# Optimization experiments

Measured on AMD Instinct MI355X. Metric: run time of the kernel, lower is better.

Reference implementation:

```python
import jax, jax.numpy as jnp
import numpy as np

FORGET_BIAS = 1.0  # tf.nn.rnn_cell.LSTMCell default


def _lstm_scan(x_btE, W, b, hidden):
    """x: (B,T,E). W: (E+H, 4H), gate order i, j, f, o (TF LSTMCell)."""
    B = x_btE.shape[0]
    h0 = jnp.zeros((B, hidden), x_btE.dtype)
    c0 = jnp.zeros((B, hidden), x_btE.dtype)

    def step(carry, x_t):
        h, c = carry
        z = jnp.concatenate([x_t, h], axis=-1) @ W + b  # (B, 4H)
        i, j, f, o = jnp.split(z, 4, axis=-1)
        c_new = jax.nn.sigmoid(f + FORGET_BIAS) * c + jax.nn.sigmoid(i) * jnp.tanh(j)
        h_new = jax.nn.sigmoid(o) * jnp.tanh(c_new)
        return (h_new, c_new), h_new

    (_, _), hs = jax.lax.scan(step, (h0, c0), jnp.swapaxes(x_btE, 0, 1))
    return jnp.swapaxes(hs, 0, 1)  # (B, T, H)


def setup_inputs() -> dict:
    key = jax.random.key(0)
    ks = jax.random.split(key, 5)
    B, T, V, E, H, C = 256, 120, 50000, 256, 1024, 5
    tokens = jax.random.randint(ks[0], (B, T, 1), 0, V, dtype=jnp.int32)
    embeddings = jax.random.normal(ks[1], (V, E), jnp.float32) * 0.1
    W_lstm = jax.random.normal(ks[2], (E + H, 4 * H), jnp.float32) * (1.0 / np.sqrt(E + H))
    b_lstm = jnp.zeros((4 * H,), jnp.float32)
    U = jax.random.normal(ks[3], (H, C), jnp.float32) * (1.0 / np.sqrt(H))
    b2 = jnp.zeros((C,), jnp.float32)
    return {"tokens": tokens, "embeddings": embeddings, "W_lstm": W_lstm,
            "b_lstm": b_lstm, "U": U, "b2": b2}


def reference(tokens, embeddings, W_lstm, b_lstm, U, b2):
    B, T, F = tokens.shape  # F == n_features == 1
    E = embeddings.shape[1]
    H = U.shape[0]
    # embedding lookup + reshape to (B, T, F*E)
    x = embeddings[tokens].reshape(B, T, F * E)
    outputs = _lstm_scan(x, W_lstm, b_lstm, H)  # (B, T, H); dropout keep_prob=1 -> identity
    preds = outputs.reshape(-1, H) @ U + b2
    return preds.reshape(B, T, -1)  # (B, max_length, n_classes)
```

## Files before the change

### kernel.cpp

```cpp
#include <hip/hip_runtime.h>

typedef unsigned short u16;
typedef unsigned int u32;
typedef unsigned long long u64;
typedef int   v4i  __attribute__((ext_vector_type(4)));
typedef short v8s  __attribute__((ext_vector_type(8)));
typedef float v2f  __attribute__((ext_vector_type(2)));
typedef float v16f __attribute__((ext_vector_type(16)));

#define B_ 256
#define T_ 120
#define E_ 256
#define H_ 1024
#define K_ 1280
#define LDH 1032
#define LDX 264

#define WS_WF   0
#define WS_X    10485760
#define WS_HS   26214400
#define WS_BAR  89128960

__device__ __forceinline__ u16 f2bf(float f) {
    union { float f; u32 u; } v; v.f = f;
    u32 r = v.u + 0x7fffu + ((v.u >> 16) & 1u);
    return (u16)(r >> 16);
}
__device__ __forceinline__ float bf2f(u16 u) {
    union { u32 u; float f; } v; v.u = ((u32)u) << 16; return v.f;
}
__device__ __forceinline__ float fsig(float x) {
    float t = __builtin_amdgcn_exp2f(-1.44269504f * x);
    return __builtin_amdgcn_rcpf(1.0f + t);
}
__device__ __forceinline__ float ftanh_(float x) {
    float xc = fminf(8.0f, fmaxf(-8.0f, x));
    float t = __builtin_amdgcn_exp2f(2.88539008f * xc);
    return (t - 1.0f) * __builtin_amdgcn_rcpf(t + 1.0f);
}
__device__ __forceinline__ void gl_lds16(const void* g, void* l) {
    __builtin_amdgcn_global_load_lds(
        (const __attribute__((address_space(1))) void*)g,
        (__attribute__((address_space(3))) void*)l, 16, 0, 0);
}

__global__ void prep_w(const float* __restrict__ W, u16* __restrict__ Wf) {
    __shared__ u16 tile[32 * 136];
    int bid = blockIdx.x;
    int cid = bid / 5, fo = bid % 5;
    int kh  = cid & 1, g = (cid >> 1) & 3, nc = cid >> 3;
    int colbase = g * 1024 + nc * 32;
    int tid = threadIdx.x;
    int c = tid & 31, r = tid >> 5;

#pragma unroll
    for (int fl = 0; fl < 8; ++fl) {
        int k0 = (2 * (fo * 8 + fl) + kh) * 16;
#pragma unroll
        for (int rr = 0; rr < 2; ++rr) {
            int row = r + rr * 8;
            float v = W[(size_t)(k0 + row) * 4096 + colbase + c];
            tile[c * 136 + fl * 16 + row] = f2bf(v);
        }
    }
    __syncthreads();

    int lane = tid & 63;
#pragma unroll
    for (int pass = 0; pass < 2; ++pass) {
        int fl = (tid >> 6) + pass * 4;
        v4i o = *(const v4i*)&tile[(lane & 31) * 136 + fl * 16 + ((lane >> 5) << 3)];
        *(v4i*)(Wf + (((size_t)(cid * 40 + fo * 8 + fl)) << 9) + lane * 8) = o;
    }
}

__global__ void prep_x(const int* __restrict__ tokens, const float* __restrict__ emb,
                       u16* __restrict__ X) {
    int v   = blockIdx.x * 256 + threadIdx.x;
    int e8  = v & 31;
    int row = v >> 5;
    int t = row >> 8, b = row & 255;
    int tok = tokens[b * T_ + t];
    const float* src = emb + (size_t)tok * E_ + e8 * 8;
    u16 o[8];
#pragma unroll
    for (int j = 0; j < 8; ++j) o[j] = f2bf(src[j]);
    *(v4i*)(X + (size_t)row * E_ + e8 * 8) = *(v4i*)o;
}

__global__ __launch_bounds__(512, 2) void lstm_main(
    const u16* __restrict__ Wf, const u16* __restrict__ X,
    const float* __restrict__ b_lstm, u16* __restrict__ hs,
    u32* __restrict__ bar) {

    __shared__ u16  hbuf[32 * LDH];
    __shared__ u16  xbuf[32 * LDX];
    __shared__ float gates[2 * 4 * 32 * 34];
    __shared__ float bias[128];

    const int tid   = threadIdx.x;
    const int lane  = tid & 63;
    const int wv    = tid >> 6;
    const int g     = wv >> 1;
    const int khalf = wv & 1;
    const int bid   = blockIdx.x;
    const int mchunk = bid & 7;
    const int nc    = bid >> 3;
    const int m0    = mchunk << 5;

    if (tid < 128) bias[tid] = b_lstm[(tid >> 5) * H_ + (nc << 5) + (tid & 31)];

    v8s Wr[40];
    {
        const int cid = nc * 8 + g * 2 + khalf;
        const v4i* wsrc = (const v4i*)(Wf + (size_t)cid * 40 * 512);
#pragma unroll
        for (int f = 0; f < 40; ++f)
            Wr[f] = __builtin_bit_cast(v8s, wsrc[f * 64 + lane]);
    }
#pragma unroll
    for (int f = 0; f < 40; ++f) asm volatile("" : "+v"(Wr[f]));

    {
        const v4i* xs = (const v4i*)(X + (size_t)m0 * E_);
#pragma unroll
        for (int i = 0; i < 2; ++i) {
            int idx = tid + i * 512;
            int r = idx >> 5, c8 = idx & 31;
            *(v4i*)&xbuf[r * LDX + c8 * 8] = xs[r * 32 + c8];
        }
    }
    __syncthreads();

    const u16* Ax = &xbuf[(lane & 31) * LDX + ((lane >> 5) << 3)];
    const u16* Ah = &hbuf[(lane & 31) * LDH + ((lane >> 5) << 3)];

    v16f acc = {0,0,0,0,0,0,0,0,0,0,0,0,0,0,0,0};
#pragma unroll
    for (int f = 0; f < 8; ++f) {
        v8s a = *(const v8s*)(Ax + (2 * f + khalf) * 16);
        acc = __builtin_amdgcn_mfma_f32_32x32x16_bf16(a, Wr[f], acc, 0, 0, 0);
    }

    float cst[2] = {0.f, 0.f};
    const int cm  = tid >> 4;
    const int cn2 = (tid & 15) << 1;
    u32* hs32 = (u32*)hs;

    for (int t = 0; t < T_; ++t) {
        if (t > 0) {
            if (tid == 0) {
                u32* p = &bar[mchunk * T_ + (t - 1)];
                while (__hip_atomic_load(p, __ATOMIC_RELAXED, __HIP_MEMORY_SCOPE_AGENT) < 32u)
                    __builtin_amdgcn_s_sleep(1);
            }
            __syncthreads();
            {
                const u16* srcb = hs + ((size_t)(t - 1) * B_ + m0) * H_;
                int r0 = wv << 2;
#pragma unroll
                for (int half = 0; half < 2; ++half)
#pragma unroll
                    for (int i = 0; i < 4; ++i) {
                        int r = r0 + i;
                        gl_lds16(srcb + (size_t)r * H_ + half * 512 + lane * 8,
                                 &hbuf[r * LDH + half * 512]);
                    }
            }
            asm volatile("s_waitcnt vmcnt(4)\n\ts_barrier" ::: "memory");
#pragma unroll
            for (int f = 8; f < 24; ++f) {
                v8s a = *(const v8s*)(Ah + ((2 * f + khalf) * 16 - 256));
                acc = __builtin_amdgcn_mfma_f32_32x32x16_bf16(a, Wr[f], acc, 0, 0, 0);
            }
            asm volatile("s_waitcnt vmcnt(0)\n\ts_barrier" ::: "memory");
#pragma unroll
            for (int f = 24; f < 40; ++f) {
                v8s a = *(const v8s*)(Ah + ((2 * f + khalf) * 16 - 256));
                acc = __builtin_amdgcn_mfma_f32_32x32x16_bf16(a, Wr[f], acc, 0, 0, 0);
            }
        }

        {
            float* gb = &gates[((khalf << 2) + g) * 1088];
            int col = lane & 31, rq = (lane >> 5) << 2;
#pragma unroll
            for (int reg = 0; reg < 16; ++reg) {
                int row = (reg & 3) + ((reg >> 2) << 3) + rq;
                gb[row * 34 + col] = acc[reg];
            }
        }
        __syncthreads();

        if (t + 1 < T_) {
            const v4i* xs = (const v4i*)(X + ((size_t)(t + 1) * B_ + m0) * E_);
#pragma unroll
            for (int i = 0; i < 2; ++i) {
                int idx = tid + i * 512;
                int r = idx >> 5, c8 = idx & 31;
                *(v4i*)&xbuf[r * LDX + c8 * 8] = xs[r * 32 + c8];
            }
        }

        u32 hpack = 0;
        {
            v2f zz[4];
#pragma unroll
            for (int gg = 0; gg < 4; ++gg) {
                v2f a = *(const v2f*)&gates[gg * 1088 + cm * 34 + cn2];
                v2f b = *(const v2f*)&gates[(4 + gg) * 1088 + cm * 34 + cn2];
                zz[gg].x = a.x + b.x; zz[gg].y = a.y + b.y;
            }
#pragma unroll
            for (int q = 0; q < 2; ++q) {
                int n = cn2 + q;
                float ip = zz[0][q] + bias[n];
                float jp = zz[1][q] + bias[32 + n];
                float fp = zz[2][q] + bias[64 + n] + 1.0f;
                float op = zz[3][q] + bias[96 + n];
                float cc = fsig(fp) * cst[q] + fsig(ip) * ftanh_(jp);
                cst[q] = cc;
                hpack |= ((u32)f2bf(fsig(op) * ftanh_(cc))) << (16 * q);
            }
        }
        __hip_atomic_store(&hs32[((size_t)t * B_ + m0 + cm) * 512 + (nc << 4) + (tid & 15)],
                           hpack, __ATOMIC_RELAXED, __HIP_MEMORY_SCOPE_AGENT);

        if (t + 1 < T_) {
            asm volatile("s_waitcnt vmcnt(0)" ::: "memory");
            __syncthreads();
            if (tid == 0)
                __hip_atomic_fetch_add(&bar[mchunk * T_ + t], 1u,
                                       __ATOMIC_RELAXED, __HIP_MEMORY_SCOPE_AGENT);
#pragma unroll
            for (int reg = 0; reg < 16; ++reg) acc[reg] = 0.f;
#pragma unroll
            for (int f = 0; f < 8; ++f) {
                v8s a = *(const v8s*)(Ax + (2 * f + khalf) * 16);
                acc = __builtin_amdgcn_mfma_f32_32x32x16_bf16(a, Wr[f], acc, 0, 0, 0);
            }
        }
    }
}

__global__ void proj_kernel(const u16* __restrict__ hs, const float* __restrict__ U,
                            const float* __restrict__ b2, float* __restrict__ out) {
    __shared__ float Ul[H_ * 5];
    int tid = threadIdx.x;
    for (int i = tid; i < H_ * 5; i += 256) Ul[i] = U[i];
    __syncthreads();
    int wv = tid >> 6, lane = tid & 63;
#pragma unroll 1
    for (int i = 0; i < 16; ++i) {
        int row = blockIdx.x * 64 + wv * 16 + i;
        int t = row >> 8, b = row & 255;
        const v4i* hp = (const v4i*)(hs + (size_t)row * H_);
        float p[5] = {0.f, 0.f, 0.f, 0.f, 0.f};
#pragma unroll
        for (int half = 0; half < 2; ++half) {
            v4i hv = hp[lane * 2 + half];
            u16 us[8];
            *(v4i*)us = hv;
#pragma unroll
            for (int j = 0; j < 8; ++j) {
                float hf = bf2f(us[j]);
                int k = lane * 16 + half * 8 + j;
#pragma unroll
                for (int c = 0; c < 5; ++c) p[c] += hf * Ul[k * 5 + c];
            }
        }
#pragma unroll
        for (int c = 0; c < 5; ++c)
            for (int off = 32; off > 0; off >>= 1)
                p[c] += __shfl_down(p[c], off, 64);
        if (lane == 0) {
#pragma unroll
            for (int c = 0; c < 5; ++c)
                out[((size_t)b * T_ + t) * 5 + c] = p[c] + b2[c];
        }
    }
}

extern "C" void kernel_launch(void* const* d_in, const int* in_sizes, int n_in,
                              void* d_out, int out_size, void* d_ws, size_t ws_size,
                              hipStream_t stream) {
    const int*   tokens = (const int*)d_in[0];
    const float* emb    = (const float*)d_in[1];
    const float* W      = (const float*)d_in[2];
    const float* b_l    = (const float*)d_in[3];
    const float* U      = (const float*)d_in[4];
    const float* b2     = (const float*)d_in[5];
    float* out = (float*)d_out;

    char* ws = (char*)d_ws;
    u16* Wf  = (u16*)(ws + WS_WF);
    u16* X   = (u16*)(ws + WS_X);
    u16* hs  = (u16*)(ws + WS_HS);
    u32* bar = (u32*)(ws + WS_BAR);

    hipMemsetAsync(bar, 0, 8 * T_ * sizeof(u32), stream);
    prep_w<<<1280, 256, 0, stream>>>(W, Wf);
    prep_x<<<3840, 256, 0, stream>>>(tokens, emb, X);
    lstm_main<<<256, 512, 0, stream>>>(Wf, X, b_l, hs, bar);
    proj_kernel<<<480, 256, 0, stream>>>(hs, U, b2, out);
}
```

Measured before the change: 607.9 us.

## Split LSTM step barrier into per-half flags and restructure wave K/N split

Each wave now owns two gate column tiles and a quarter of K instead of one gate and half of K, so the prepacked weight layout and the gate reduction change to four partial sums. The per-timestep barrier counter is split into two flags, one per half of the hidden dimension, so each block can start loading the first half of h while the second half is still being produced. The input-projection MFMAs are moved to after the wait, overlapping with the asynchronous h loads. This aims to shorten the serial critical path per step, at the cost of more LDS for gate partials and every thread spin-polling the flags instead of a single thread.

```diff
diff --git a/kernel.cpp b/kernel.cpp
--- a/kernel.cpp
+++ b/kernel.cpp
@@ -45,32 +45,33 @@
 }
 
 __global__ void prep_w(const float* __restrict__ W, u16* __restrict__ Wf) {
-    __shared__ u16 tile[32 * 136];
+    __shared__ u16 tile[64 * 72];
     int bid = blockIdx.x;
     int cid = bid / 5, fo = bid % 5;
-    int kh  = cid & 1, g = (cid >> 1) & 3, nc = cid >> 3;
-    int colbase = g * 1024 + nc * 32;
+    int kq  = cid & 3, np = (cid >> 2) & 1, nc = cid >> 3;
     int tid = threadIdx.x;
-    int c = tid & 31, r = tid >> 5;
-
-#pragma unroll
-    for (int fl = 0; fl < 8; ++fl) {
-        int k0 = (2 * (fo * 8 + fl) + kh) * 16;
-#pragma unroll
-        for (int rr = 0; rr < 2; ++rr) {
-            int row = r + rr * 8;
-            float v = W[(size_t)(k0 + row) * 4096 + colbase + c];
-            tile[c * 136 + fl * 16 + row] = f2bf(v);
+    int cc = tid & 31, n = (tid >> 5) & 1, r = tid >> 6;
+
+    int col = (np * 2 + n) * 1024 + nc * 32 + cc;
+#pragma unroll
+    for (int fl = 0; fl < 4; ++fl) {
+        int k0 = (4 * (fo * 4 + fl) + kq) * 16;
+#pragma unroll
+        for (int rr = 0; rr < 4; ++rr) {
+            int krow = rr * 4 + r;
+            float v = W[(size_t)(k0 + krow) * 4096 + col];
+            tile[(n * 32 + cc) * 72 + fl * 16 + krow] = f2bf(v);
         }
     }
     __syncthreads();
 
-    int lane = tid & 63;
+    int lane = tid & 63, wvv = tid >> 6;
 #pragma unroll
     for (int pass = 0; pass < 2; ++pass) {
-        int fl = (tid >> 6) + pass * 4;
-        v4i o = *(const v4i*)&tile[(lane & 31) * 136 + fl * 16 + ((lane >> 5) << 3)];
-        *(v4i*)(Wf + (((size_t)(cid * 40 + fo * 8 + fl)) << 9) + lane * 8) = o;
+        int slot = wvv + pass * 4;
+        int fl = slot >> 1, nn = slot & 1;
+        v4i o = *(const v4i*)&tile[(nn * 32 + (lane & 31)) * 72 + fl * 16 + ((lane >> 5) << 3)];
+        *(v4i*)(Wf + (size_t)cid * 20480 + (((fo * 4 + fl) * 2 + nn) << 9) + lane * 8) = o;
     }
 }
 
@@ -95,31 +96,36 @@
 
     __shared__ u16  hbuf[32 * LDH];
     __shared__ u16  xbuf[32 * LDX];
-    __shared__ float gates[2 * 4 * 32 * 34];
+    __shared__ float gates[4 * 4 * 32 * 34];
     __shared__ float bias[128];
 
     const int tid   = threadIdx.x;
     const int lane  = tid & 63;
     const int wv    = tid >> 6;
-    const int g     = wv >> 1;
-    const int khalf = wv & 1;
+    const int np    = wv >> 2;
+    const int kq    = wv & 3;
     const int bid   = blockIdx.x;
     const int mchunk = bid & 7;
     const int nc    = bid >> 3;
     const int m0    = mchunk << 5;
+    const int hl    = nc >> 4;
 
     if (tid < 128) bias[tid] = b_lstm[(tid >> 5) * H_ + (nc << 5) + (tid & 31)];
 
-    v8s Wr[40];
+    v8s Wr[20][2];
     {
-        const int cid = nc * 8 + g * 2 + khalf;
-        const v4i* wsrc = (const v4i*)(Wf + (size_t)cid * 40 * 512);
-#pragma unroll
-        for (int f = 0; f < 40; ++f)
-            Wr[f] = __builtin_bit_cast(v8s, wsrc[f * 64 + lane]);
-    }
-#pragma unroll
-    for (int f = 0; f < 40; ++f) asm volatile("" : "+v"(Wr[f]));
+        const v4i* wsrc = (const v4i*)(Wf + (size_t)(nc * 8 + np * 4 + kq) * 20480);
+#pragma unroll
+        for (int f = 0; f < 20; ++f)
+#pragma unroll
+            for (int n = 0; n < 2; ++n)
+                Wr[f][n] = __builtin_bit_cast(v8s, wsrc[(f * 2 + n) * 64 + lane]);
+    }
+#pragma unroll
+    for (int f = 0; f < 20; ++f) {
+        asm volatile("" : "+v"(Wr[f][0]));
+        asm volatile("" : "+v"(Wr[f][1]));
+    }
 
     {
         const v4i* xs = (const v4i*)(X + (size_t)m0 * E_);
@@ -135,59 +141,69 @@
     const u16* Ax = &xbuf[(lane & 31) * LDX + ((lane >> 5) << 3)];
     const u16* Ah = &hbuf[(lane & 31) * LDH + ((lane >> 5) << 3)];
 
-    v16f acc = {0,0,0,0,0,0,0,0,0,0,0,0,0,0,0,0};
-#pragma unroll
-    for (int f = 0; f < 8; ++f) {
-        v8s a = *(const v8s*)(Ax + (2 * f + khalf) * 16);
-        acc = __builtin_amdgcn_mfma_f32_32x32x16_bf16(a, Wr[f], acc, 0, 0, 0);
-    }
-
     float cst[2] = {0.f, 0.f};
     const int cm  = tid >> 4;
     const int cn2 = (tid & 15) << 1;
     u32* hs32 = (u32*)hs;
 
     for (int t = 0; t < T_; ++t) {
+        v16f acc0 = {0,0,0,0,0,0,0,0,0,0,0,0,0,0,0,0};
+        v16f acc1 = {0,0,0,0,0,0,0,0,0,0,0,0,0,0,0,0};
+
         if (t > 0) {
-            if (tid == 0) {
-                u32* p = &bar[mchunk * T_ + (t - 1)];
-                while (__hip_atomic_load(p, __ATOMIC_RELAXED, __HIP_MEMORY_SCOPE_AGENT) < 32u)
-                    __builtin_amdgcn_s_sleep(1);
-            }
-            __syncthreads();
-            {
-                const u16* srcb = hs + ((size_t)(t - 1) * B_ + m0) * H_;
-                int r0 = wv << 2;
-#pragma unroll
-                for (int half = 0; half < 2; ++half)
-#pragma unroll
-                    for (int i = 0; i < 4; ++i) {
-                        int r = r0 + i;
-                        gl_lds16(srcb + (size_t)r * H_ + half * 512 + lane * 8,
-                                 &hbuf[r * LDH + half * 512]);
-                    }
+            const u32* flg = &bar[((size_t)mchunk * T_ + (t - 1)) * 2];
+            const u16* srcb = hs + ((size_t)(t - 1) * B_ + m0) * H_;
+            const int r0 = wv << 2;
+            while (__hip_atomic_load(&flg[0], __ATOMIC_RELAXED, __HIP_MEMORY_SCOPE_AGENT) < 16u)
+                __builtin_amdgcn_s_sleep(1);
+#pragma unroll
+            for (int i = 0; i < 4; ++i)
+                gl_lds16(srcb + (size_t)(r0 + i) * H_ + lane * 8,
+                         &hbuf[(r0 + i) * LDH]);
+            while (__hip_atomic_load(&flg[1], __ATOMIC_RELAXED, __HIP_MEMORY_SCOPE_AGENT) < 16u)
+                __builtin_amdgcn_s_sleep(1);
+#pragma unroll
+            for (int i = 0; i < 4; ++i)
+                gl_lds16(srcb + (size_t)(r0 + i) * H_ + 512 + lane * 8,
+                         &hbuf[(r0 + i) * LDH + 512]);
+#pragma unroll
+            for (int f = 0; f < 4; ++f) {
+                v8s a = *(const v8s*)(Ax + (4 * f + kq) * 16);
+                acc0 = __builtin_amdgcn_mfma_f32_32x32x16_bf16(a, Wr[f][0], acc0, 0, 0, 0);
+                acc1 = __builtin_amdgcn_mfma_f32_32x32x16_bf16(a, Wr[f][1], acc1, 0, 0, 0);
             }
             asm volatile("s_waitcnt vmcnt(4)\n\ts_barrier" ::: "memory");
 #pragma unroll
-            for (int f = 8; f < 24; ++f) {
-                v8s a = *(const v8s*)(Ah + ((2 * f + khalf) * 16 - 256));
-                acc = __builtin_amdgcn_mfma_f32_32x32x16_bf16(a, Wr[f], acc, 0, 0, 0);
+            for (int f = 4; f < 12; ++f) {
+                v8s a = *(const v8s*)(Ah + (4 * f + kq) * 16 - 256);
+                acc0 = __builtin_amdgcn_mfma_f32_32x32x16_bf16(a, Wr[f][0], acc0, 0, 0, 0);
+                acc1 = __builtin_amdgcn_mfma_f32_32x32x16_bf16(a, Wr[f][1], acc1, 0, 0, 0);
             }
             asm volatile("s_waitcnt vmcnt(0)\n\ts_barrier" ::: "memory");
 #pragma unroll
-            for (int f = 24; f < 40; ++f) {
-                v8s a = *(const v8s*)(Ah + ((2 * f + khalf) * 16 - 256));
-                acc = __builtin_amdgcn_mfma_f32_32x32x16_bf16(a, Wr[f], acc, 0, 0, 0);
+            for (int f = 12; f < 20; ++f) {
+                v8s a = *(const v8s*)(Ah + (4 * f + kq) * 16 - 256);
+                acc0 = __builtin_amdgcn_mfma_f32_32x32x16_bf16(a, Wr[f][0], acc0, 0, 0, 0);
+                acc1 = __builtin_amdgcn_mfma_f32_32x32x16_bf16(a, Wr[f][1], acc1, 0, 0, 0);
+            }
+        } else {
+#pragma unroll
+            for (int f = 0; f < 4; ++f) {
+                v8s a = *(const v8s*)(Ax + (4 * f + kq) * 16);
+                acc0 = __builtin_amdgcn_mfma_f32_32x32x16_bf16(a, Wr[f][0], acc0, 0, 0, 0);
+                acc1 = __builtin_amdgcn_mfma_f32_32x32x16_bf16(a, Wr[f][1], acc1, 0, 0, 0);
             }
         }
 
         {
-            float* gb = &gates[((khalf << 2) + g) * 1088];
             int col = lane & 31, rq = (lane >> 5) << 2;
+            float* g0 = &gates[(kq * 4 + np * 2 + 0) * 1088];
+            float* g1 = &gates[(kq * 4 + np * 2 + 1) * 1088];
 #pragma unroll
             for (int reg = 0; reg < 16; ++reg) {
                 int row = (reg & 3) + ((reg >> 2) << 3) + rq;
-                gb[row * 34 + col] = acc[reg];
+                g0[row * 34 + col] = acc0[reg];
+                g1[row * 34 + col] = acc1[reg];
             }
         }
         __syncthreads();
@@ -207,9 +223,12 @@
             v2f zz[4];
 #pragma unroll
             for (int gg = 0; gg < 4; ++gg) {
-                v2f a = *(const v2f*)&gates[gg * 1088 + cm * 34 + cn2];
-                v2f b = *(const v2f*)&gates[(4 + gg) * 1088 + cm * 34 + cn2];
-                zz[gg].x = a.x + b.x; zz[gg].y = a.y + b.y;
+                v2f s0 = *(const v2f*)&gates[(0 * 4 + gg) * 1088 + cm * 34 + cn2];
+                v2f s1 = *(const v2f*)&gates[(1 * 4 + gg) * 1088 + cm * 34 + cn2];
+                v2f s2 = *(const v2f*)&gates[(2 * 4 + gg) * 1088 + cm * 34 + cn2];
+                v2f s3 = *(const v2f*)&gates[(3 * 4 + gg) * 1088 + cm * 34 + cn2];
+                zz[gg].x = (s0.x + s1.x) + (s2.x + s3.x);
+                zz[gg].y = (s0.y + s1.y) + (s2.y + s3.y);
             }
 #pragma unroll
             for (int q = 0; q < 2; ++q) {
@@ -230,15 +249,8 @@
             asm volatile("s_waitcnt vmcnt(0)" ::: "memory");
             __syncthreads();
             if (tid == 0)
-                __hip_atomic_fetch_add(&bar[mchunk * T_ + t], 1u,
+                __hip_atomic_fetch_add(&bar[((size_t)mchunk * T_ + t) * 2 + hl], 1u,
                                        __ATOMIC_RELAXED, __HIP_MEMORY_SCOPE_AGENT);
-#pragma unroll
-            for (int reg = 0; reg < 16; ++reg) acc[reg] = 0.f;
-#pragma unroll
-            for (int f = 0; f < 8; ++f) {
-                v8s a = *(const v8s*)(Ax + (2 * f + khalf) * 16);
-                acc = __builtin_amdgcn_mfma_f32_32x32x16_bf16(a, Wr[f], acc, 0, 0, 0);
-            }
         }
     }
 }
@@ -298,7 +310,7 @@
     u16* hs  = (u16*)(ws + WS_HS);
     u32* bar = (u32*)(ws + WS_BAR);
 
-    hipMemsetAsync(bar, 0, 8 * T_ * sizeof(u32), stream);
+    hipMemsetAsync(bar, 0, 8 * T_ * 2 * sizeof(u32), stream);
     prep_w<<<1280, 256, 0, stream>>>(W, Wf);
     prep_x<<<3840, 256, 0, stream>>>(tokens, emb, X);
     lstm_main<<<256, 512, 0, stream>>>(Wf, X, b_l, hs, bar);
```

New measurement: 1.201 ms. 97.6% more time.

## Fuse projection into LSTM kernel, merge prep kernels, use per-block barrier flags

Applied to the files above, without the earlier changes.

Merges the weight, embedding and output-bias prep into one launch, and removes the separate projection kernel. Each block now projects its h slice onto U in registers and accumulates into the output with atomicAdd, which avoids re-reading all hidden states. The inter-block barrier changes from one counter with atomic adds to 32 per-producer flags that 32 threads poll in parallel. This adds global atomics and an unconditional barrier plus vmcnt wait on every step, and the order of the float atomic sums is nondeterministic.

```diff
diff --git a/kernel.cpp b/kernel.cpp
--- a/kernel.cpp
+++ b/kernel.cpp
@@ -12,7 +12,6 @@
 #define T_ 120
 #define E_ 256
 #define H_ 1024
-#define K_ 1280
 #define LDH 1032
 #define LDX 264
 
@@ -26,9 +25,6 @@
     u32 r = v.u + 0x7fffu + ((v.u >> 16) & 1u);
     return (u16)(r >> 16);
 }
-__device__ __forceinline__ float bf2f(u16 u) {
-    union { u32 u; float f; } v; v.u = ((u32)u) << 16; return v.f;
-}
 __device__ __forceinline__ float fsig(float x) {
     float t = __builtin_amdgcn_exp2f(-1.44269504f * x);
     return __builtin_amdgcn_rcpf(1.0f + t);
@@ -44,54 +40,61 @@
         (__attribute__((address_space(3))) void*)l, 16, 0, 0);
 }
 
-__global__ void prep_w(const float* __restrict__ W, u16* __restrict__ Wf) {
+__global__ void prep_all(const float* __restrict__ W, u16* __restrict__ Wf,
+                         const int* __restrict__ tokens, const float* __restrict__ emb,
+                         u16* __restrict__ X, const float* __restrict__ b2,
+                         float* __restrict__ out) {
     __shared__ u16 tile[32 * 136];
     int bid = blockIdx.x;
-    int cid = bid / 5, fo = bid % 5;
-    int kh  = cid & 1, g = (cid >> 1) & 3, nc = cid >> 3;
-    int colbase = g * 1024 + nc * 32;
     int tid = threadIdx.x;
-    int c = tid & 31, r = tid >> 5;
-
-#pragma unroll
-    for (int fl = 0; fl < 8; ++fl) {
-        int k0 = (2 * (fo * 8 + fl) + kh) * 16;
-#pragma unroll
-        for (int rr = 0; rr < 2; ++rr) {
-            int row = r + rr * 8;
-            float v = W[(size_t)(k0 + row) * 4096 + colbase + c];
-            tile[c * 136 + fl * 16 + row] = f2bf(v);
-        }
-    }
-    __syncthreads();
-
-    int lane = tid & 63;
-#pragma unroll
-    for (int pass = 0; pass < 2; ++pass) {
-        int fl = (tid >> 6) + pass * 4;
-        v4i o = *(const v4i*)&tile[(lane & 31) * 136 + fl * 16 + ((lane >> 5) << 3)];
-        *(v4i*)(Wf + (((size_t)(cid * 40 + fo * 8 + fl)) << 9) + lane * 8) = o;
-    }
-}
-
-__global__ void prep_x(const int* __restrict__ tokens, const float* __restrict__ emb,
-                       u16* __restrict__ X) {
-    int v   = blockIdx.x * 256 + threadIdx.x;
-    int e8  = v & 31;
-    int row = v >> 5;
-    int t = row >> 8, b = row & 255;
-    int tok = tokens[b * T_ + t];
-    const float* src = emb + (size_t)tok * E_ + e8 * 8;
-    u16 o[8];
-#pragma unroll
-    for (int j = 0; j < 8; ++j) o[j] = f2bf(src[j]);
-    *(v4i*)(X + (size_t)row * E_ + e8 * 8) = *(v4i*)o;
+    if (bid < 1280) {
+        int cid = bid / 5, fo = bid % 5;
+        int kh  = cid & 1, g = (cid >> 1) & 3, nc = cid >> 3;
+        int colbase = g * 1024 + nc * 32;
+        int c = tid & 31, r = tid >> 5;
+#pragma unroll
+        for (int fl = 0; fl < 8; ++fl) {
+            int k0 = (2 * (fo * 8 + fl) + kh) * 16;
+#pragma unroll
+            for (int rr = 0; rr < 2; ++rr) {
+                int row = r + rr * 8;
+                float v = W[(size_t)(k0 + row) * 4096 + colbase + c];
+                tile[c * 136 + fl * 16 + row] = f2bf(v);
+            }
+        }
+        __syncthreads();
+        int lane = tid & 63;
+#pragma unroll
+        for (int pass = 0; pass < 2; ++pass) {
+            int fl = (tid >> 6) + pass * 4;
+            v4i o = *(const v4i*)&tile[(lane & 31) * 136 + fl * 16 + ((lane >> 5) << 3)];
+            *(v4i*)(Wf + (((size_t)(cid * 40 + fo * 8 + fl)) << 9) + lane * 8) = o;
+        }
+    } else if (bid < 5120) {
+        int v   = (bid - 1280) * 256 + tid;
+        int e8  = v & 31;
+        int row = v >> 5;
+        int t = row >> 8, b = row & 255;
+        int tok = tokens[b * T_ + t];
+        const float* src = emb + (size_t)tok * E_ + e8 * 8;
+        u16 o[8];
+#pragma unroll
+        for (int j = 0; j < 8; ++j) o[j] = f2bf(src[j]);
+        *(v4i*)(X + (size_t)row * E_ + e8 * 8) = *(v4i*)o;
+    } else {
+        int row = (bid - 5120) * 256 + tid;
+        if (row < B_ * T_) {
+#pragma unroll
+            for (int c = 0; c < 5; ++c) out[(size_t)row * 5 + c] = b2[c];
+        }
+    }
 }
 
 __global__ __launch_bounds__(512, 2) void lstm_main(
     const u16* __restrict__ Wf, const u16* __restrict__ X,
     const float* __restrict__ b_lstm, u16* __restrict__ hs,
-    u32* __restrict__ bar) {
+    u32* __restrict__ bar, const float* __restrict__ U,
+    float* __restrict__ out) {
 
     __shared__ u16  hbuf[32 * LDH];
     __shared__ u16  xbuf[32 * LDX];
@@ -112,14 +115,22 @@
 
     v8s Wr[40];
     {
-        const int cid = nc * 8 + g * 2 + khalf;
-        const v4i* wsrc = (const v4i*)(Wf + (size_t)cid * 40 * 512);
+        const v4i* wsrc = (const v4i*)(Wf + (size_t)(nc * 8 + g * 2 + khalf) * 20480);
 #pragma unroll
         for (int f = 0; f < 40; ++f)
             Wr[f] = __builtin_bit_cast(v8s, wsrc[f * 64 + lane]);
     }
 #pragma unroll
     for (int f = 0; f < 40; ++f) asm volatile("" : "+v"(Wr[f]));
+
+    const int cm  = tid >> 4;
+    const int cn2 = (tid & 15) << 1;
+    float Ur[2][5];
+#pragma unroll
+    for (int q = 0; q < 2; ++q)
+#pragma unroll
+        for (int c = 0; c < 5; ++c)
+            Ur[q][c] = U[(size_t)((nc << 5) + cn2 + q) * 5 + c];
 
     {
         const v4i* xs = (const v4i*)(X + (size_t)m0 * E_);
@@ -143,46 +154,44 @@
     }
 
     float cst[2] = {0.f, 0.f};
-    const int cm  = tid >> 4;
-    const int cn2 = (tid & 15) << 1;
     u32* hs32 = (u32*)hs;
 
     for (int t = 0; t < T_; ++t) {
         if (t > 0) {
-            if (tid == 0) {
-                u32* p = &bar[mchunk * T_ + (t - 1)];
-                while (__hip_atomic_load(p, __ATOMIC_RELAXED, __HIP_MEMORY_SCOPE_AGENT) < 32u)
+            if (tid < 32) {
+                u32* p = &bar[(size_t)((mchunk * T_ + (t - 1)) << 5) + tid];
+                while (!__hip_atomic_load(p, __ATOMIC_RELAXED, __HIP_MEMORY_SCOPE_AGENT))
                     __builtin_amdgcn_s_sleep(1);
             }
             __syncthreads();
             {
                 const u16* srcb = hs + ((size_t)(t - 1) * B_ + m0) * H_;
-                int r0 = wv << 2;
-#pragma unroll
-                for (int half = 0; half < 2; ++half)
-#pragma unroll
-                    for (int i = 0; i < 4; ++i) {
-                        int r = r0 + i;
-                        gl_lds16(srcb + (size_t)r * H_ + half * 512 + lane * 8,
-                                 &hbuf[r * LDH + half * 512]);
-                    }
+                const int r0 = wv << 2;
+#pragma unroll
+                for (int i = 0; i < 4; ++i)
+                    gl_lds16(srcb + (size_t)(r0 + i) * H_ + lane * 8,
+                             &hbuf[(r0 + i) * LDH]);
+#pragma unroll
+                for (int i = 0; i < 4; ++i)
+                    gl_lds16(srcb + (size_t)(r0 + i) * H_ + 512 + lane * 8,
+                             &hbuf[(r0 + i) * LDH + 512]);
             }
             asm volatile("s_waitcnt vmcnt(4)\n\ts_barrier" ::: "memory");
 #pragma unroll
             for (int f = 8; f < 24; ++f) {
-                v8s a = *(const v8s*)(Ah + ((2 * f + khalf) * 16 - 256));
+                v8s a = *(const v8s*)(Ah + (2 * f + khalf) * 16 - 256);
                 acc = __builtin_amdgcn_mfma_f32_32x32x16_bf16(a, Wr[f], acc, 0, 0, 0);
             }
             asm volatile("s_waitcnt vmcnt(0)\n\ts_barrier" ::: "memory");
 #pragma unroll
             for (int f = 24; f < 40; ++f) {
-                v8s a = *(const v8s*)(Ah + ((2 * f + khalf) * 16 - 256));
+                v8s a = *(const v8s*)(Ah + (2 * f + khalf) * 16 - 256);
                 acc = __builtin_amdgcn_mfma_f32_32x32x16_bf16(a, Wr[f], acc, 0, 0, 0);
             }
         }
 
         {
-            float* gb = &gates[((khalf << 2) + g) * 1088];
+            float* gb = &gates[(khalf * 4 + g) * 1088];
             int col = lane & 31, rq = (lane >> 5) << 2;
 #pragma unroll
             for (int reg = 0; reg < 16; ++reg) {
@@ -202,7 +211,7 @@
             }
         }
 
-        u32 hpack = 0;
+        float hh[2];
         {
             v2f zz[4];
 #pragma unroll
@@ -211,6 +220,7 @@
                 v2f b = *(const v2f*)&gates[(4 + gg) * 1088 + cm * 34 + cn2];
                 zz[gg].x = a.x + b.x; zz[gg].y = a.y + b.y;
             }
+            u32 hpack = 0;
 #pragma unroll
             for (int q = 0; q < 2; ++q) {
                 int n = cn2 + q;
@@ -220,18 +230,19 @@
                 float op = zz[3][q] + bias[96 + n];
                 float cc = fsig(fp) * cst[q] + fsig(ip) * ftanh_(jp);
                 cst[q] = cc;
-                hpack |= ((u32)f2bf(fsig(op) * ftanh_(cc))) << (16 * q);
-            }
-        }
-        __hip_atomic_store(&hs32[((size_t)t * B_ + m0 + cm) * 512 + (nc << 4) + (tid & 15)],
-                           hpack, __ATOMIC_RELAXED, __HIP_MEMORY_SCOPE_AGENT);
-
+                hh[q] = fsig(op) * ftanh_(cc);
+                hpack |= ((u32)f2bf(hh[q])) << (16 * q);
+            }
+            __hip_atomic_store(&hs32[((size_t)t * B_ + m0 + cm) * 512 + (nc << 4) + (tid & 15)],
+                               hpack, __ATOMIC_RELAXED, __HIP_MEMORY_SCOPE_AGENT);
+        }
+
+        asm volatile("s_waitcnt vmcnt(0)" ::: "memory");
+        __syncthreads();
         if (t + 1 < T_) {
-            asm volatile("s_waitcnt vmcnt(0)" ::: "memory");
-            __syncthreads();
             if (tid == 0)
-                __hip_atomic_fetch_add(&bar[mchunk * T_ + t], 1u,
-                                       __ATOMIC_RELAXED, __HIP_MEMORY_SCOPE_AGENT);
+                __hip_atomic_store(&bar[(size_t)((mchunk * T_ + t) << 5) + nc], 1u,
+                                   __ATOMIC_RELAXED, __HIP_MEMORY_SCOPE_AGENT);
 #pragma unroll
             for (int reg = 0; reg < 16; ++reg) acc[reg] = 0.f;
 #pragma unroll
@@ -240,43 +251,25 @@
                 acc = __builtin_amdgcn_mfma_f32_32x32x16_bf16(a, Wr[f], acc, 0, 0, 0);
             }
         }
-    }
-}
-
-__global__ void proj_kernel(const u16* __restrict__ hs, const float* __restrict__ U,
-                            const float* __restrict__ b2, float* __restrict__ out) {
-    __shared__ float Ul[H_ * 5];
-    int tid = threadIdx.x;
-    for (int i = tid; i < H_ * 5; i += 256) Ul[i] = U[i];
-    __syncthreads();
-    int wv = tid >> 6, lane = tid & 63;
-#pragma unroll 1
-    for (int i = 0; i < 16; ++i) {
-        int row = blockIdx.x * 64 + wv * 16 + i;
-        int t = row >> 8, b = row & 255;
-        const v4i* hp = (const v4i*)(hs + (size_t)row * H_);
-        float p[5] = {0.f, 0.f, 0.f, 0.f, 0.f};
-#pragma unroll
-        for (int half = 0; half < 2; ++half) {
-            v4i hv = hp[lane * 2 + half];
-            u16 us[8];
-            *(v4i*)us = hv;
-#pragma unroll
-            for (int j = 0; j < 8; ++j) {
-                float hf = bf2f(us[j]);
-                int k = lane * 16 + half * 8 + j;
-#pragma unroll
-                for (int c = 0; c < 5; ++c) p[c] += hf * Ul[k * 5 + c];
-            }
-        }
-#pragma unroll
-        for (int c = 0; c < 5; ++c)
-            for (int off = 32; off > 0; off >>= 1)
-                p[c] += __shfl_down(p[c], off, 64);
-        if (lane == 0) {
+
+        {
+            float p[5];
 #pragma unroll
             for (int c = 0; c < 5; ++c)
-                out[((size_t)b * T_ + t) * 5 + c] = p[c] + b2[c];
+                p[c] = hh[0] * Ur[0][c] + hh[1] * Ur[1][c];
+#pragma unroll
+            for (int c = 0; c < 5; ++c) {
+                p[c] += __shfl_xor(p[c], 1, 16);
+                p[c] += __shfl_xor(p[c], 2, 16);
+                p[c] += __shfl_xor(p[c], 4, 16);
+                p[c] += __shfl_xor(p[c], 8, 16);
+            }
+            if ((tid & 15) == 0) {
+                float* dst = &out[((size_t)(m0 + cm) * T_ + t) * 5];
+#pragma unroll
+                for (int c = 0; c < 5; ++c)
+                    atomicAdd(dst + c, p[c]);
+            }
         }
     }
 }
@@ -298,9 +291,7 @@
     u16* hs  = (u16*)(ws + WS_HS);
     u32* bar = (u32*)(ws + WS_BAR);
 
-    hipMemsetAsync(bar, 0, 8 * T_ * sizeof(u32), stream);
-    prep_w<<<1280, 256, 0, stream>>>(W, Wf);
-    prep_x<<<3840, 256, 0, stream>>>(tokens, emb, X);
-    lstm_main<<<256, 512, 0, stream>>>(Wf, X, b_l, hs, bar);
-    proj_kernel<<<480, 256, 0, stream>>>(hs, U, b2, out);
-}
+    hipMemsetAsync(bar, 0, 8 * T_ * 32 * sizeof(u32), stream);
+    prep_all<<<5240, 256, 0, stream>>>(W, Wf, tokens, emb, X, b2, out);
+    lstm_main<<<256, 512, 0, stream>>>(Wf, X, b_l, hs, bar, U, out);
+}
```

New measurement: 928.7 us. 52.8% more time.

## Replace atomic-counter barrier with per-block flags and merge prep kernels

Applied to the files above, without the earlier changes.

The per-step grid barrier now uses one flag slot per producer block, set with plain atomic stores, and 32 threads each poll one flag. This replaces a single counter hit by 32 atomic fetch-adds. The memset and the two prep kernels are folded into one prep_all launch that also zeroes the enlarged flag array, removing two launches. The cost is more flag memory and wider polling traffic in each step.

```diff
diff --git a/kernel.cpp b/kernel.cpp
--- a/kernel.cpp
+++ b/kernel.cpp
@@ -2,7 +2,6 @@
 
 typedef unsigned short u16;
 typedef unsigned int u32;
-typedef unsigned long long u64;
 typedef int   v4i  __attribute__((ext_vector_type(4)));
 typedef short v8s  __attribute__((ext_vector_type(8)));
 typedef float v2f  __attribute__((ext_vector_type(2)));
@@ -12,7 +11,6 @@
 #define T_ 120
 #define E_ 256
 #define H_ 1024
-#define K_ 1280
 #define LDH 1032
 #define LDX 264
 
@@ -44,48 +42,50 @@
         (__attribute__((address_space(3))) void*)l, 16, 0, 0);
 }
 
-__global__ void prep_w(const float* __restrict__ W, u16* __restrict__ Wf) {
+__global__ void prep_all(const float* __restrict__ W, u16* __restrict__ Wf,
+                         const int* __restrict__ tokens, const float* __restrict__ emb,
+                         u16* __restrict__ X, u32* __restrict__ bar) {
     __shared__ u16 tile[32 * 136];
     int bid = blockIdx.x;
-    int cid = bid / 5, fo = bid % 5;
-    int kh  = cid & 1, g = (cid >> 1) & 3, nc = cid >> 3;
-    int colbase = g * 1024 + nc * 32;
     int tid = threadIdx.x;
-    int c = tid & 31, r = tid >> 5;
-
-#pragma unroll
-    for (int fl = 0; fl < 8; ++fl) {
-        int k0 = (2 * (fo * 8 + fl) + kh) * 16;
-#pragma unroll
-        for (int rr = 0; rr < 2; ++rr) {
-            int row = r + rr * 8;
-            float v = W[(size_t)(k0 + row) * 4096 + colbase + c];
-            tile[c * 136 + fl * 16 + row] = f2bf(v);
-        }
-    }
-    __syncthreads();
-
-    int lane = tid & 63;
-#pragma unroll
-    for (int pass = 0; pass < 2; ++pass) {
-        int fl = (tid >> 6) + pass * 4;
-        v4i o = *(const v4i*)&tile[(lane & 31) * 136 + fl * 16 + ((lane >> 5) << 3)];
-        *(v4i*)(Wf + (((size_t)(cid * 40 + fo * 8 + fl)) << 9) + lane * 8) = o;
-    }
-}
-
-__global__ void prep_x(const int* __restrict__ tokens, const float* __restrict__ emb,
-                       u16* __restrict__ X) {
-    int v   = blockIdx.x * 256 + threadIdx.x;
-    int e8  = v & 31;
-    int row = v >> 5;
-    int t = row >> 8, b = row & 255;
-    int tok = tokens[b * T_ + t];
-    const float* src = emb + (size_t)tok * E_ + e8 * 8;
-    u16 o[8];
-#pragma unroll
-    for (int j = 0; j < 8; ++j) o[j] = f2bf(src[j]);
-    *(v4i*)(X + (size_t)row * E_ + e8 * 8) = *(v4i*)o;
+    if (bid < 1280) {
+        int cid = bid / 5, fo = bid % 5;
+        int kh  = cid & 1, g = (cid >> 1) & 3, nc = cid >> 3;
+        int colbase = g * 1024 + nc * 32;
+        int c = tid & 31, r = tid >> 5;
+#pragma unroll
+        for (int fl = 0; fl < 8; ++fl) {
+            int k0 = (2 * (fo * 8 + fl) + kh) * 16;
+#pragma unroll
+            for (int rr = 0; rr < 2; ++rr) {
+                int row = r + rr * 8;
+                float v = W[(size_t)(k0 + row) * 4096 + colbase + c];
+                tile[c * 136 + fl * 16 + row] = f2bf(v);
+            }
+        }
+        __syncthreads();
+        int lane = tid & 63;
+#pragma unroll
+        for (int pass = 0; pass < 2; ++pass) {
+            int fl = (tid >> 6) + pass * 4;
+            v4i o = *(const v4i*)&tile[(lane & 31) * 136 + fl * 16 + ((lane >> 5) << 3)];
+            *(v4i*)(Wf + (((size_t)(cid * 40 + fo * 8 + fl)) << 9) + lane * 8) = o;
+        }
+    } else if (bid < 5120) {
+        int v   = (bid - 1280) * 256 + tid;
+        int e8  = v & 31;
+        int row = v >> 5;
+        int t = row >> 8, b = row & 255;
+        int tok = tokens[b * T_ + t];
+        const float* src = emb + (size_t)tok * E_ + e8 * 8;
+        u16 o[8];
+#pragma unroll
+        for (int j = 0; j < 8; ++j) o[j] = f2bf(src[j]);
+        *(v4i*)(X + (size_t)row * E_ + e8 * 8) = *(v4i*)o;
+    } else {
+        int idx = (bid - 5120) * 256 + tid;
+        bar[idx] = 0u;
+    }
 }
 
 __global__ __launch_bounds__(512, 2) void lstm_main(
@@ -112,8 +112,7 @@
 
     v8s Wr[40];
     {
-        const int cid = nc * 8 + g * 2 + khalf;
-        const v4i* wsrc = (const v4i*)(Wf + (size_t)cid * 40 * 512);
+        const v4i* wsrc = (const v4i*)(Wf + (size_t)(nc * 8 + g * 2 + khalf) * 20480);
 #pragma unroll
         for (int f = 0; f < 40; ++f)
             Wr[f] = __builtin_bit_cast(v8s, wsrc[f * 64 + lane]);
@@ -149,40 +148,40 @@
 
     for (int t = 0; t < T_; ++t) {
         if (t > 0) {
-            if (tid == 0) {
-                u32* p = &bar[mchunk * T_ + (t - 1)];
-                while (__hip_atomic_load(p, __ATOMIC_RELAXED, __HIP_MEMORY_SCOPE_AGENT) < 32u)
+            if (tid < 32) {
+                u32* p = &bar[(size_t)((mchunk * T_ + (t - 1)) << 5) + tid];
+                while (!__hip_atomic_load(p, __ATOMIC_RELAXED, __HIP_MEMORY_SCOPE_AGENT))
                     __builtin_amdgcn_s_sleep(1);
             }
             __syncthreads();
             {
                 const u16* srcb = hs + ((size_t)(t - 1) * B_ + m0) * H_;
-                int r0 = wv << 2;
-#pragma unroll
-                for (int half = 0; half < 2; ++half)
-#pragma unroll
-                    for (int i = 0; i < 4; ++i) {
-                        int r = r0 + i;
-                        gl_lds16(srcb + (size_t)r * H_ + half * 512 + lane * 8,
-                                 &hbuf[r * LDH + half * 512]);
-                    }
+                const int r0 = wv << 2;
+#pragma unroll
+                for (int i = 0; i < 4; ++i)
+                    gl_lds16(srcb + (size_t)(r0 + i) * H_ + lane * 8,
+                             &hbuf[(r0 + i) * LDH]);
+#pragma unroll
+                for (int i = 0; i < 4; ++i)
+                    gl_lds16(srcb + (size_t)(r0 + i) * H_ + 512 + lane * 8,
+                             &hbuf[(r0 + i) * LDH + 512]);
             }
             asm volatile("s_waitcnt vmcnt(4)\n\ts_barrier" ::: "memory");
 #pragma unroll
             for (int f = 8; f < 24; ++f) {
-                v8s a = *(const v8s*)(Ah + ((2 * f + khalf) * 16 - 256));
+                v8s a = *(const v8s*)(Ah + (2 * f + khalf) * 16 - 256);
                 acc = __builtin_amdgcn_mfma_f32_32x32x16_bf16(a, Wr[f], acc, 0, 0, 0);
             }
             asm volatile("s_waitcnt vmcnt(0)\n\ts_barrier" ::: "memory");
 #pragma unroll
             for (int f = 24; f < 40; ++f) {
-                v8s a = *(const v8s*)(Ah + ((2 * f + khalf) * 16 - 256));
+                v8s a = *(const v8s*)(Ah + (2 * f + khalf) * 16 - 256);
                 acc = __builtin_amdgcn_mfma_f32_32x32x16_bf16(a, Wr[f], acc, 0, 0, 0);
             }
         }
 
         {
-            float* gb = &gates[((khalf << 2) + g) * 1088];
+            float* gb = &gates[(khalf * 4 + g) * 1088];
             int col = lane & 31, rq = (lane >> 5) << 2;
 #pragma unroll
             for (int reg = 0; reg < 16; ++reg) {
@@ -230,8 +229,8 @@
             asm volatile("s_waitcnt vmcnt(0)" ::: "memory");
             __syncthreads();
             if (tid == 0)
-                __hip_atomic_fetch_add(&bar[mchunk * T_ + t], 1u,
-                                       __ATOMIC_RELAXED, __HIP_MEMORY_SCOPE_AGENT);
+                __hip_atomic_store(&bar[(size_t)((mchunk * T_ + t) << 5) + nc], 1u,
+                                   __ATOMIC_RELAXED, __HIP_MEMORY_SCOPE_AGENT);
 #pragma unroll
             for (int reg = 0; reg < 16; ++reg) acc[reg] = 0.f;
 #pragma unroll
@@ -298,9 +297,7 @@
     u16* hs  = (u16*)(ws + WS_HS);
     u32* bar = (u32*)(ws + WS_BAR);
 
-    hipMemsetAsync(bar, 0, 8 * T_ * sizeof(u32), stream);
-    prep_w<<<1280, 256, 0, stream>>>(W, Wf);
-    prep_x<<<3840, 256, 0, stream>>>(tokens, emb, X);
+    prep_all<<<5240, 256, 0, stream>>>(W, Wf, tokens, emb, X, bar);
     lstm_main<<<256, 512, 0, stream>>>(Wf, X, b_l, hs, bar);
     proj_kernel<<<480, 256, 0, stream>>>(hs, U, b2, out);
 }
```

After: 615.2 us. Within noise of the previous version (+1.2%).
